# Kernel optimization log

Hardware: AMD Instinct MI355X
Metric: run time of the kernel (lower is better)

Reference implementation:

```python
import jax, jax.numpy as jnp
import numpy as np

N = 50000      # nodes
E = 800000     # edges
F_IN = 128     # input features
H = 64         # hidden channels
G = 64         # graphs in batch
EPS = 1e-5


def setup_inputs() -> dict:
    key = jax.random.key(0)
    ks = jax.random.split(key, 24)
    def nrm(k, s):
        return jax.random.normal(k, s, dtype=jnp.float32) * 0.05
    inp = {
        "x": nrm(ks[0], (N, F_IN)),
        "edge_index": jax.random.randint(ks[1], (2, E), 0, N),
        "batch": jnp.sort(jax.random.randint(ks[2], (N,), 0, G)),
        # GCNConv weights (stored [in, out]; math equivalent to torch Linear)
        "W0": nrm(ks[3], (F_IN, H)), "b0": nrm(ks[4], (H,)),
        "W1": nrm(ks[5], (H, H)),    "b1": nrm(ks[6], (H,)),
        "W2": nrm(ks[7], (H, H)),    "b2": nrm(ks[8], (H,)),
        # residual linears
        "RW0": nrm(ks[9], (F_IN, H)),  "rb0": nrm(ks[10], (H,)),
        "RW1": nrm(ks[11], (H, H)),    "rb1": nrm(ks[12], (H,)),
        "RW2": nrm(ks[13], (H, H)),    "rb2": nrm(ks[14], (H,)),
        # layernorm gamma/beta
        "g0": jnp.ones((H,), jnp.float32), "be0": jnp.zeros((H,), jnp.float32),
        "g1": jnp.ones((H,), jnp.float32), "be1": jnp.zeros((H,), jnp.float32),
        "g2": jnp.ones((H,), jnp.float32), "be2": jnp.zeros((H,), jnp.float32),
        # final readout linear
        "lw": nrm(ks[15], (H, 1)), "lb": nrm(ks[16], (1,)),
    }
    return inp


def _layernorm(x, g, b):
    mu = jnp.mean(x, axis=-1, keepdims=True)
    var = jnp.mean(jnp.square(x - mu), axis=-1, keepdims=True)
    return (x - mu) * jax.lax.rsqrt(var + EPS) * g + b


def reference(x, edge_index, batch,
              W0, b0, W1, b1, W2, b2,
              RW0, rb0, RW1, rb1, RW2, rb2,
              g0, be0, g1, be1, g2, be2,
              lw, lb):
    n = x.shape[0]
    loops = jnp.arange(n)
    row = jnp.concatenate([edge_index[0], loops])  # source
    col = jnp.concatenate([edge_index[1], loops])  # target
    # symmetric GCN normalization with self-loops (PyG gcn_norm)
    deg = jax.ops.segment_sum(jnp.ones_like(col, dtype=x.dtype), col, num_segments=n)
    dis = jnp.where(deg > 0, deg ** -0.5, 0.0)
    norm = dis[row] * dis[col]  # [E+N]

    params = [(W0, b0, RW0, rb0, g0, be0),
              (W1, b1, RW1, rb1, g1, be1),
              (W2, b2, RW2, rb2, g2, be2)]
    n_layers = len(params)
    for i, (W, b, RW, rb, g, be) in enumerate(params):
        h = x @ W                                                  # [n, H]
        agg = jax.ops.segment_sum(h[row] * norm[:, None], col, num_segments=n) + b
        x = agg + (x @ RW + rb)                                    # residual
        # dropout: eval mode -> identity
        x = _layernorm(x, g, be)
        if i < n_layers - 1:
            x = jax.nn.relu(x)

    # global mean pool over graphs
    counts = jax.ops.segment_sum(jnp.ones((n,), x.dtype), batch, num_segments=G)
    pooled = jax.ops.segment_sum(x, batch, num_segments=G) / jnp.maximum(counts, 1.0)[:, None]
    return pooled @ lw + lb  # [G, 1]
```

## Files before the change

kernel.cpp:

```cpp
#include <hip/hip_runtime.h>
#include <hip/hip_bf16.h>

#define HID 64
#define NGRAPH 64
#define BSH 7
#define NCH 384

static inline size_t align256(size_t x) { return (x + 255) & ~(size_t)255; }

typedef __attribute__((ext_vector_type(8))) short bf16x8;
typedef __attribute__((ext_vector_type(4))) float f32x4;

__device__ __forceinline__ float ldf(const void* p, size_t i, int f32) {
    if (f32) return ((const float*)p)[i];
    unsigned int w = ((unsigned int)((const unsigned short*)p)[i]) << 16;
    return __uint_as_float(w);
}
__device__ __forceinline__ float bf2f(unsigned short u) {
    return __uint_as_float(((unsigned int)u) << 16);
}
__device__ __forceinline__ unsigned short f2bf(float f) {
    __hip_bfloat16 h = __float2bfloat16(f);
    return *(unsigned short*)&h;
}

__device__ __forceinline__ unsigned char f2e4m3(float f) {
#if defined(__has_builtin) && __has_builtin(__builtin_amdgcn_cvt_pk_fp8_f32)
    int r = __builtin_amdgcn_cvt_pk_fp8_f32(f, f, 0, false);
    return (unsigned char)(r & 0xFF);
#else
    unsigned u = __float_as_uint(f);
    unsigned s = (u >> 24) & 0x80;
    unsigned a = u & 0x7FFFFFFF;
    float af = __uint_as_float(a);
    if (af < 0.015625f) {
        int m = (int)rintf(af * 512.f);
        return (unsigned char)(s | m);
    }
    unsigned r = a + 0x7FFFF + ((a >> 20) & 1);
    int e = (int)(r >> 23) - 127;
    if (e > 8) return (unsigned char)(s | 0x7E);
    return (unsigned char)(s | ((e + 7) << 3) | ((r >> 20) & 7));
#endif
}
template <int IDX>
__device__ __forceinline__ float d8(unsigned p) {
#if defined(__has_builtin) && __has_builtin(__builtin_amdgcn_cvt_f32_fp8)
    return __builtin_amdgcn_cvt_f32_fp8(p, IDX);
#else
    unsigned b = (p >> (IDX * 8)) & 0xFF;
    unsigned e = (b >> 3) & 0xF, m = b & 7;
    float v = e ? __uint_as_float(((e + 120) << 23) | (m << 20))
                : (float)m * (1.f / 512.f);
    return (b & 0x80) ? -v : v;
#endif
}

__global__ void k_sniff(const unsigned short* __restrict__ x, int nwords, int* __restrict__ flag,
                        float* __restrict__ gsum, int* __restrict__ gcnt) {
    __shared__ int cw, cz;
    int t = threadIdx.x;
    if (t == 0) { cw = 0; cz = 0; }
    if (t < NGRAPH) { gsum[t] = 0.f; gcnt[t] = 0; }
    __syncthreads();
    int weird = 0, evenzero = 0;
    for (int i = t; i < nwords; i += blockDim.x) {
        unsigned short u = x[i];
        int e = (u >> 7) & 0xFF;
        if (e >= 128) weird++;
        if (((i & 1) == 0) && ((u & 0x7FFF) == 0)) evenzero++;
    }
    atomicAdd(&cw, weird);
    atomicAdd(&cz, evenzero);
    __syncthreads();
    if (t == 0) *flag = (cw > nwords / 16 || cz > nwords / 8) ? 1 : 0;
}

__global__ void k_gcnt(const int* __restrict__ batch, int* __restrict__ gcnt, int n) {
    __shared__ int h[NGRAPH];
    int t = threadIdx.x;
    if (t < NGRAPH) h[t] = 0;
    __syncthreads();
    int i = blockIdx.x * blockDim.x + t;
    if (i < n) atomicAdd(&h[batch[i]], 1);
    __syncthreads();
    if (t < NGRAPH && h[t] > 0) atomicAdd(&gcnt[t], h[t]);
}

__global__ void k_pack(const void* W0, const void* RW0, const void* b0, const void* rb0,
                       const void* W1, const void* RW1, const void* b1, const void* rb1,
                       const void* W2, const void* RW2, const void* b2, const void* rb2,
                       const int* __restrict__ dflag,
                       unsigned short* wt0, unsigned short* wt1, unsigned short* wt2,
                       float* bcat) {
    int f = *dflag;
    int i = blockIdx.x * blockDim.x + threadIdx.x;
    if (i < 16384) {
        int n = i >> 7, k = i & 127;
        float v = (n < 64) ? ldf(W0, (size_t)k * 64 + n, f) : ldf(RW0, (size_t)k * 64 + (n - 64), f);
        wt0[n * 128 + k] = f2bf(v);
    } else if (i < 24576) {
        int j = i - 16384; int n = j >> 6, k = j & 63;
        float v = (n < 64) ? ldf(W1, (size_t)k * 64 + n, f) : ldf(RW1, (size_t)k * 64 + (n - 64), f);
        wt1[n * 64 + k] = f2bf(v);
    } else if (i < 32768) {
        int j = i - 24576; int n = j >> 6, k = j & 63;
        float v = (n < 64) ? ldf(W2, (size_t)k * 64 + n, f) : ldf(RW2, (size_t)k * 64 + (n - 64), f);
        wt2[n * 64 + k] = f2bf(v);
    } else if (i < 32768 + 192) {
        int j = i - 32768; int l = j >> 6, c = j & 63;
        const void* bb = (l == 0) ? b0 : (l == 1) ? b1 : b2;
        const void* rr = (l == 0) ? rb0 : (l == 1) ? rb1 : rb2;
        bcat[l * 64 + c] = ldf(bb, c, f) + ldf(rr, c, f);
    }
}

__global__ __launch_bounds__(256) void k_hist(const int* __restrict__ ecol, int e, int nbuck,
                                              int* __restrict__ hist) {
    __shared__ int sh[1024];
    int c = blockIdx.x, t = threadIdx.x;
    for (int i = t; i < nbuck; i += 256) sh[i] = 0;
    __syncthreads();
    int per = (e + NCH - 1) / NCH;
    int s = c * per, en = min(e, s + per);
    for (int i = s + t; i < en; i += 256)
        atomicAdd(&sh[ecol[i] >> BSH], 1);
    __syncthreads();
    for (int i = t; i < nbuck; i += 256) hist[i * NCH + c] = sh[i];
}

__global__ void k_scan1(const int* __restrict__ src, int* __restrict__ bsum, int n) {
    __shared__ int s[256];
    int t = threadIdx.x;
    int base = blockIdx.x * 1024 + t * 4;
    int sum = 0;
#pragma unroll
    for (int j = 0; j < 4; j++) { int i = base + j; if (i < n) sum += src[i]; }
    s[t] = sum;
    __syncthreads();
    for (int o = 128; o > 0; o >>= 1) {
        if (t < o) s[t] += s[t + o];
        __syncthreads();
    }
    if (t == 0) bsum[blockIdx.x] = s[0];
}

__global__ void k_scan2(const int* __restrict__ bsum, int* __restrict__ bscan,
                        int* __restrict__ out, int nb, int n) {
    __shared__ int s[256];
    int t = threadIdx.x;
    int v = (t < nb) ? bsum[t] : 0;
    s[t] = v;
    __syncthreads();
    for (int o = 1; o < 256; o <<= 1) {
        int x = (t >= o) ? s[t - o] : 0;
        __syncthreads();
        s[t] += x;
        __syncthreads();
    }
    if (t < nb) bscan[t] = s[t] - v;
    if (t == nb - 1) out[n] = s[t];
}

__global__ void k_scan3(const int* __restrict__ src, const int* __restrict__ bscan,
                        int* __restrict__ out, int n) {
    __shared__ int s[256];
    int t = threadIdx.x;
    int base = blockIdx.x * 1024 + t * 4;
    int tsum = 0;
#pragma unroll
    for (int j = 0; j < 4; j++) { int i = base + j; if (i < n) tsum += src[i]; }
    s[t] = tsum;
    __syncthreads();
    for (int o = 1; o < 256; o <<= 1) {
        int x = (t >= o) ? s[t - o] : 0;
        __syncthreads();
        s[t] += x;
        __syncthreads();
    }
    int off = bscan[blockIdx.x] + s[t] - tsum;
#pragma unroll
    for (int j = 0; j < 4; j++) {
        int i = base + j;
        if (i < n) { out[i] = off; off += src[i]; }
    }
}

__global__ __launch_bounds__(256) void k_scatter(const int* __restrict__ erow,
                                                 const int* __restrict__ ecol, int e, int nbuck,
                                                 const int* __restrict__ hoffs,
                                                 int2* __restrict__ ebuf) {
    __shared__ int cur[1024];
    int c = blockIdx.x, t = threadIdx.x;
    for (int i = t; i < nbuck; i += 256) cur[i] = hoffs[i * NCH + c];
    __syncthreads();
    int per = (e + NCH - 1) / NCH;
    int s = c * per, en = min(e, s + per);
    for (int i = s + t; i < en; i += 256) {
        int tg = ecol[i];
        int p = atomicAdd(&cur[tg >> BSH], 1);
        ebuf[p] = make_int2(erow[i], tg);
    }
}

__global__ __launch_bounds__(256) void k_bucket(const int2* __restrict__ ebuf,
                                                const int* __restrict__ hoffs,
                                                int nbuck, int n, int e,
                                                int* __restrict__ offs, float* __restrict__ dis,
                                                int* __restrict__ csr) {
    __shared__ int hist[128];
    __shared__ int lofs[128];
    __shared__ int curs[128];
    int b = blockIdx.x, t = threadIdx.x;
    int nb0 = b << BSH;
    int nn = n - nb0; if (nn > 128) nn = 128;
    int s = hoffs[b * NCH];
    int en = (b + 1 < nbuck) ? hoffs[(b + 1) * NCH] : e;
    if (t < 128) hist[t] = 0;
    __syncthreads();
    for (int i = s + t; i < en; i += 256)
        atomicAdd(&hist[ebuf[i].y & 127], 1);
    __syncthreads();
    if (t < 128) lofs[t] = hist[t];
    __syncthreads();
    for (int o = 1; o < 128; o <<= 1) {
        int v = (t < 128 && t >= o) ? lofs[t - o] : 0;
        __syncthreads();
        if (t < 128) lofs[t] += v;
        __syncthreads();
    }
    if (t < nn) {
        int ex = s + lofs[t] - hist[t];
        offs[nb0 + t] = ex;
        curs[t] = ex;
        dis[nb0 + t] = rsqrtf((float)(hist[t] + 1));
    }
    if (b == nbuck - 1 && t == 0) offs[n] = e;
    __syncthreads();
    for (int i = s + t; i < en; i += 256) {
        int2 ed = ebuf[i];
        int p = atomicAdd(&curs[ed.y & 127], 1);
        csr[p] = ed.x;
    }
}

template <int K, bool XFLAG, bool LO>
__global__ __launch_bounds__(256) void k_gemm(const void* __restrict__ xin,
                                              const unsigned short* __restrict__ wt,
                                              const float* __restrict__ bcat,
                                              const float* __restrict__ dis,
                                              const int* __restrict__ dflag,
                                              unsigned char* __restrict__ hs,
                                              float* __restrict__ base, int n) {
    const int KP = K + 8;
    __shared__ unsigned short sXh[64 * KP];
    __shared__ unsigned short sXl[LO ? 64 * KP : 1];
    __shared__ unsigned short sW[128 * KP];
    int f32 = *dflag;
    int tid = threadIdx.x;
    int row0 = blockIdx.x * 64;

    {
        const uint4* src = (const uint4*)wt;
        uint4* dst = (uint4*)sW;
        const int C = K / 8;
        const int CP = KP / 8;
        for (int i = tid; i < 128 * C; i += 256) {
            int nrow = i / C, c = i % C;
            dst[nrow * CP + c] = src[i];
        }
    }
    if (XFLAG && !f32) {
        const uint4* xv = (const uint4*)xin;
        const int C = K / 8;
        for (int i = tid; i < 64 * C; i += 256) {
            int r = i / C, c = i % C;
            int gr = row0 + r;
            uint4 v = (gr < n) ? xv[(size_t)gr * C + c] : make_uint4(0, 0, 0, 0);
            *(uint4*)&sXh[r * KP + c * 8] = v;
        }
    } else if (XFLAG) {
        for (int i = tid; i < 64 * K; i += 256) {
            int r = i / K, k = i - r * K;
            int gr = row0 + r;
            float v = (gr < n) ? ((const float*)xin)[(size_t)gr * K + k] : 0.f;
            sXh[r * KP + k] = f2bf(v);
        }
    } else {
        const float4* xv = (const float4*)xin;
        const int C = K / 4;
        for (int i = tid; i < 64 * C; i += 256) {
            int r = i / C, c = i % C;
            int gr = row0 + r;
            float4 v = (gr < n) ? xv[(size_t)gr * C + c] : make_float4(0.f, 0.f, 0.f, 0.f);
            ushort4 h, lo;
            h.x = f2bf(v.x); h.y = f2bf(v.y); h.z = f2bf(v.z); h.w = f2bf(v.w);
            if (LO) {
                lo.x = f2bf(v.x - bf2f(h.x)); lo.y = f2bf(v.y - bf2f(h.y));
                lo.z = f2bf(v.z - bf2f(h.z)); lo.w = f2bf(v.w - bf2f(h.w));
            }
            *(ushort4*)&sXh[r * KP + c * 4] = h;
            if (LO) *(ushort4*)&sXl[r * KP + c * 4] = lo;
        }
    }
    __syncthreads();

    int w = tid >> 6, lane = tid & 63;
    int m = lane & 15, q = lane >> 4;
    f32x4 acc[8];
#pragma unroll
    for (int ct = 0; ct < 8; ct++) acc[ct] = (f32x4){0.f, 0.f, 0.f, 0.f};

    int arow = w * 16 + m;
#pragma unroll
    for (int ks = 0; ks < K / 32; ks++) {
        int ka = ks * 32 + q * 8;
        bf16x8 ah = *(const bf16x8*)&sXh[arow * KP + ka];
        bf16x8 al;
        if (LO) al = *(const bf16x8*)&sXl[arow * KP + ka];
#pragma unroll
        for (int ct = 0; ct < 8; ct++) {
            bf16x8 bb = *(const bf16x8*)&sW[(ct * 16 + m) * KP + ka];
            acc[ct] = __builtin_amdgcn_mfma_f32_16x16x32_bf16(ah, bb, acc[ct], 0, 0, 0);
            if (LO) acc[ct] = __builtin_amdgcn_mfma_f32_16x16x32_bf16(al, bb, acc[ct], 0, 0, 0);
        }
    }

#pragma unroll
    for (int ct = 0; ct < 4; ct++) {
        int col = ct * 16 + m;
#pragma unroll
        for (int reg = 0; reg < 4; reg++) {
            int r = row0 + w * 16 + q * 4 + reg;
            if (r < n) {
                float dv = dis[r];
                float h = acc[ct][reg] * dv;
                hs[(size_t)r * 64 + col] = f2e4m3(h);
                base[(size_t)r * 64 + col] = h * dv + acc[ct + 4][reg] + bcat[col];
            }
        }
    }
}

template <bool FINAL>
__global__ __launch_bounds__(1024) void k_agg_ln(const unsigned char* __restrict__ hs,
                                                 const float* __restrict__ base,
                                                 const float* __restrict__ dis,
                                                 const int* __restrict__ offs,
                                                 const int* __restrict__ csr,
                                                 const void* __restrict__ gam,
                                                 const void* __restrict__ bet,
                                                 const int* __restrict__ dflag,
                                                 float* __restrict__ xout, int n, int relu,
                                                 const int* __restrict__ batch,
                                                 const void* __restrict__ lw,
                                                 float* __restrict__ gsum) {
    __shared__ float sG[FINAL ? NGRAPH : 1];
    int f32 = *dflag;
    int t = threadIdx.x;
    if (FINAL) {
        if (t < NGRAPH) sG[t] = 0.f;
        __syncthreads();
    }
    int grp = t >> 4;
    int l = t & 15;
    int gl0 = (t & 63) & ~15;
    int v = blockIdx.x * 64 + grp;
    if (v < n) {
        int s = offs[v];
        int e2 = offs[v + 1];
        float a0 = 0.f, a1 = 0.f, a2 = 0.f, a3 = 0.f;
        for (int gbase = s; gbase < e2; gbase += 16) {
            int cnt = e2 - gbase; if (cnt > 16) cnt = 16;
            int myidx = (gbase + l < e2) ? csr[gbase + l] : 0;
            int j = 0;
            for (; j + 3 < cnt; j += 4) {
                int s0 = __shfl(myidx, gl0 + j, 64);
                int s1 = __shfl(myidx, gl0 + j + 1, 64);
                int s2 = __shfl(myidx, gl0 + j + 2, 64);
                int s3 = __shfl(myidx, gl0 + j + 3, 64);
                unsigned p0 = *(const unsigned*)(hs + (size_t)s0 * 64 + l * 4);
                unsigned p1 = *(const unsigned*)(hs + (size_t)s1 * 64 + l * 4);
                unsigned p2 = *(const unsigned*)(hs + (size_t)s2 * 64 + l * 4);
                unsigned p3 = *(const unsigned*)(hs + (size_t)s3 * 64 + l * 4);
                a0 += (d8<0>(p0) + d8<0>(p1)) + (d8<0>(p2) + d8<0>(p3));
                a1 += (d8<1>(p0) + d8<1>(p1)) + (d8<1>(p2) + d8<1>(p3));
                a2 += (d8<2>(p0) + d8<2>(p1)) + (d8<2>(p2) + d8<2>(p3));
                a3 += (d8<3>(p0) + d8<3>(p1)) + (d8<3>(p2) + d8<3>(p3));
            }
            for (; j < cnt; j++) {
                int s0 = __shfl(myidx, gl0 + j, 64);
                unsigned p0 = *(const unsigned*)(hs + (size_t)s0 * 64 + l * 4);
                a0 += d8<0>(p0);
                a1 += d8<1>(p0);
                a2 += d8<2>(p0);
                a3 += d8<3>(p0);
            }
        }
        float4 bv = *(const float4*)&base[(size_t)v * 64 + l * 4];
        float dv = dis[v];
        a0 = bv.x + dv * a0;
        a1 = bv.y + dv * a1;
        a2 = bv.z + dv * a2;
        a3 = bv.w + dv * a3;
        float m = a0 + a1 + a2 + a3;
        m += __shfl_xor(m, 1, 64); m += __shfl_xor(m, 2, 64);
        m += __shfl_xor(m, 4, 64); m += __shfl_xor(m, 8, 64);
        m *= (1.f / 64.f);
        float d0 = a0 - m, d1 = a1 - m, d2 = a2 - m, d3 = a3 - m;
        float var = d0 * d0 + d1 * d1 + d2 * d2 + d3 * d3;
        var += __shfl_xor(var, 1, 64); var += __shfl_xor(var, 2, 64);
        var += __shfl_xor(var, 4, 64); var += __shfl_xor(var, 8, 64);
        var *= (1.f / 64.f);
        float rs = rsqrtf(var + 1e-5f);
        float y0 = d0 * rs * ldf(gam, l * 4 + 0, f32) + ldf(bet, l * 4 + 0, f32);
        float y1 = d1 * rs * ldf(gam, l * 4 + 1, f32) + ldf(bet, l * 4 + 1, f32);
        float y2 = d2 * rs * ldf(gam, l * 4 + 2, f32) + ldf(bet, l * 4 + 2, f32);
        float y3 = d3 * rs * ldf(gam, l * 4 + 3, f32) + ldf(bet, l * 4 + 3, f32);
        if (relu) {
            y0 = fmaxf(y0, 0.f); y1 = fmaxf(y1, 0.f);
            y2 = fmaxf(y2, 0.f); y3 = fmaxf(y3, 0.f);
        }
        if (!FINAL) {
            *(float4*)&xout[(size_t)v * 64 + l * 4] = make_float4(y0, y1, y2, y3);
        } else {
            float val = y0 * ldf(lw, l * 4 + 0, f32) + y1 * ldf(lw, l * 4 + 1, f32)
                      + y2 * ldf(lw, l * 4 + 2, f32) + y3 * ldf(lw, l * 4 + 3, f32);
            val += __shfl_xor(val, 1, 64); val += __shfl_xor(val, 2, 64);
            val += __shfl_xor(val, 4, 64); val += __shfl_xor(val, 8, 64);
            if (l == 0) atomicAdd(&sG[batch[v]], val);
        }
    }
    if (FINAL) {
        __syncthreads();
        if (t < NGRAPH && sG[t] != 0.f) atomicAdd(&gsum[t], sG[t]);
    }
}

__global__ void k_final(const float* __restrict__ gsum, const int* __restrict__ gcnt,
                        const void* __restrict__ lb, const int* __restrict__ dflag,
                        void* __restrict__ out, int g) {
    int f32 = *dflag;
    int i = threadIdx.x;
    if (i < g) {
        float c = fmaxf((float)gcnt[i], 1.f);
        float v = gsum[i] / c + ldf(lb, 0, f32);
        if (f32) ((float*)out)[i] = v;
        else ((__hip_bfloat16*)out)[i] = __float2bfloat16(v);
    }
}

extern "C" void kernel_launch(void* const* d_in, const int* in_sizes, int n_in,
                              void* d_out, int out_size, void* d_ws, size_t ws_size,
                              hipStream_t stream) {
    const void* x_in = d_in[0];
    const int* edge_index = (const int*)d_in[1];
    const int* batch = (const int*)d_in[2];
    const void *W0 = d_in[3], *b0 = d_in[4], *W1 = d_in[5], *b1 = d_in[6],
               *W2 = d_in[7], *b2 = d_in[8];
    const void *RW0 = d_in[9], *rb0 = d_in[10], *RW1 = d_in[11], *rb1 = d_in[12],
               *RW2 = d_in[13], *rb2 = d_in[14];
    const void *g0 = d_in[15], *be0 = d_in[16], *g1 = d_in[17], *be1 = d_in[18],
               *g2 = d_in[19], *be2 = d_in[20], *lw = d_in[21], *lb = d_in[22];

    const int N = in_sizes[2];
    const int E = in_sizes[1] / 2;
    const int* erow = edge_index;
    const int* ecol = edge_index + E;
    const int nbuck = (N + 127) >> BSH;
    const int T = nbuck * NCH;

    char* p = (char*)d_ws;
    size_t off = 0;
    float* dis = (float*)(p + off);  off = align256(off + (size_t)N * 4);
    int* offs = (int*)(p + off);     off = align256(off + (size_t)(N + 1) * 4);
    int* csr = (int*)(p + off);      off = align256(off + (size_t)E * 4);
    int2* ebuf = (int2*)(p + off);   off = align256(off + (size_t)E * 8);
    int* hist = (int*)(p + off);     off = align256(off + (size_t)T * 4);
    int* hoffs = (int*)(p + off);    off = align256(off + (size_t)(T + 1) * 4);
    unsigned char* hs = (unsigned char*)(p + off); off = align256(off + (size_t)N * HID);
    float* base = (float*)(p + off); off = align256(off + (size_t)N * HID * 4);
    float* xbuf = (float*)(p + off); off = align256(off + (size_t)N * HID * 4);
    unsigned short* wt0 = (unsigned short*)(p + off); off = align256(off + 16384 * 2);
    unsigned short* wt1 = (unsigned short*)(p + off); off = align256(off + 8192 * 2);
    unsigned short* wt2 = (unsigned short*)(p + off); off = align256(off + 8192 * 2);
    float* bcat = (float*)(p + off); off = align256(off + 192 * 4);
    int* bsum = (int*)(p + off);     off = align256(off + 256 * 4);
    int* bscan = (int*)(p + off);    off = align256(off + 256 * 4);
    float* gsum = (float*)(p + off); off = align256(off + NGRAPH * 4);
    int* gcnt = (int*)(p + off);     off = align256(off + NGRAPH * 4);
    int* dflag = (int*)(p + off);    off = align256(off + 4);
    (void)ws_size;

    const int TB = 256;
    int nb_n = (N + TB - 1) / TB;
    int nbT = (T + 1023) / 1024;
    int nb_gemm = (N + 63) / 64;
    int nb_agg = (N + 63) / 64;

    k_sniff<<<1, 256, 0, stream>>>((const unsigned short*)x_in, 8192, dflag, gsum, gcnt);
    k_gcnt<<<nb_n, TB, 0, stream>>>(batch, gcnt, N);
    k_pack<<<130, TB, 0, stream>>>(W0, RW0, b0, rb0, W1, RW1, b1, rb1, W2, RW2, b2, rb2,
                                   dflag, wt0, wt1, wt2, bcat);
    k_hist<<<NCH, TB, 0, stream>>>(ecol, E, nbuck, hist);
    k_scan1<<<nbT, TB, 0, stream>>>(hist, bsum, T);
    k_scan2<<<1, TB, 0, stream>>>(bsum, bscan, hoffs, nbT, T);
    k_scan3<<<nbT, TB, 0, stream>>>(hist, bscan, hoffs, T);
    k_scatter<<<NCH, TB, 0, stream>>>(erow, ecol, E, nbuck, hoffs, ebuf);
    k_bucket<<<nbuck, TB, 0, stream>>>(ebuf, hoffs, nbuck, N, E, offs, dis, csr);

    k_gemm<128, true, false><<<nb_gemm, TB, 0, stream>>>(x_in, wt0, bcat, dis, dflag, hs, base, N);
    k_agg_ln<false><<<nb_agg, 1024, 0, stream>>>(hs, base, dis, offs, csr, g0, be0, dflag,
                                                 xbuf, N, 1, nullptr, nullptr, nullptr);
    k_gemm<64, false, true><<<nb_gemm, TB, 0, stream>>>(xbuf, wt1, bcat + 64, dis, dflag, hs, base, N);
    k_agg_ln<false><<<nb_agg, 1024, 0, stream>>>(hs, base, dis, offs, csr, g1, be1, dflag,
                                                 xbuf, N, 1, nullptr, nullptr, nullptr);
    k_gemm<64, false, true><<<nb_gemm, TB, 0, stream>>>(xbuf, wt2, bcat + 128, dis, dflag, hs, base, N);
    k_agg_ln<true><<<nb_agg, 1024, 0, stream>>>(hs, base, dis, offs, csr, g2, be2, dflag,
                                                nullptr, N, 0, batch, lw, gsum);

    k_final<<<1, 64, 0, stream>>>(gsum, gcnt, lb, dflag, d_out, NGRAPH);
}
```

Before: 285.1 us.

## Fuse prep kernels, split edge buffer, read weights directly, prefetch agg indices

```diff
diff --git a/kernel.cpp b/kernel.cpp
--- a/kernel.cpp
+++ b/kernel.cpp
@@ -76,57 +76,57 @@
     if (t == 0) *flag = (cw > nwords / 16 || cz > nwords / 8) ? 1 : 0;
 }
 
-__global__ void k_gcnt(const int* __restrict__ batch, int* __restrict__ gcnt, int n) {
-    __shared__ int h[NGRAPH];
-    int t = threadIdx.x;
-    if (t < NGRAPH) h[t] = 0;
-    __syncthreads();
-    int i = blockIdx.x * blockDim.x + t;
-    if (i < n) atomicAdd(&h[batch[i]], 1);
-    __syncthreads();
-    if (t < NGRAPH && h[t] > 0) atomicAdd(&gcnt[t], h[t]);
-}
-
-__global__ void k_pack(const void* W0, const void* RW0, const void* b0, const void* rb0,
-                       const void* W1, const void* RW1, const void* b1, const void* rb1,
-                       const void* W2, const void* RW2, const void* b2, const void* rb2,
-                       const int* __restrict__ dflag,
-                       unsigned short* wt0, unsigned short* wt1, unsigned short* wt2,
-                       float* bcat) {
-    int f = *dflag;
-    int i = blockIdx.x * blockDim.x + threadIdx.x;
-    if (i < 16384) {
-        int n = i >> 7, k = i & 127;
-        float v = (n < 64) ? ldf(W0, (size_t)k * 64 + n, f) : ldf(RW0, (size_t)k * 64 + (n - 64), f);
-        wt0[n * 128 + k] = f2bf(v);
-    } else if (i < 24576) {
-        int j = i - 16384; int n = j >> 6, k = j & 63;
-        float v = (n < 64) ? ldf(W1, (size_t)k * 64 + n, f) : ldf(RW1, (size_t)k * 64 + (n - 64), f);
-        wt1[n * 64 + k] = f2bf(v);
-    } else if (i < 32768) {
-        int j = i - 24576; int n = j >> 6, k = j & 63;
-        float v = (n < 64) ? ldf(W2, (size_t)k * 64 + n, f) : ldf(RW2, (size_t)k * 64 + (n - 64), f);
-        wt2[n * 64 + k] = f2bf(v);
-    } else if (i < 32768 + 192) {
-        int j = i - 32768; int l = j >> 6, c = j & 63;
-        const void* bb = (l == 0) ? b0 : (l == 1) ? b1 : b2;
-        const void* rr = (l == 0) ? rb0 : (l == 1) ? rb1 : rb2;
-        bcat[l * 64 + c] = ldf(bb, c, f) + ldf(rr, c, f);
-    }
-}
-
-__global__ __launch_bounds__(256) void k_hist(const int* __restrict__ ecol, int e, int nbuck,
+__global__ __launch_bounds__(256) void k_prep(const int* __restrict__ batch, int* __restrict__ gcnt,
+                                              int n, int nbG,
+                                              const void* W0, const void* RW0, const void* b0, const void* rb0,
+                                              const void* W1, const void* RW1, const void* b1, const void* rb1,
+                                              const void* W2, const void* RW2, const void* b2, const void* rb2,
+                                              const int* __restrict__ dflag,
+                                              unsigned short* wt0, unsigned short* wt1, unsigned short* wt2,
+                                              float* bcat,
+                                              const int* __restrict__ ecol, int e, int nbuck,
                                               int* __restrict__ hist) {
     __shared__ int sh[1024];
-    int c = blockIdx.x, t = threadIdx.x;
-    for (int i = t; i < nbuck; i += 256) sh[i] = 0;
-    __syncthreads();
-    int per = (e + NCH - 1) / NCH;
-    int s = c * per, en = min(e, s + per);
-    for (int i = s + t; i < en; i += 256)
-        atomicAdd(&sh[ecol[i] >> BSH], 1);
-    __syncthreads();
-    for (int i = t; i < nbuck; i += 256) hist[i * NCH + c] = sh[i];
+    int b = blockIdx.x, t = threadIdx.x;
+    if (b < nbG) {
+        if (t < NGRAPH) sh[t] = 0;
+        __syncthreads();
+        int i = b * 256 + t;
+        if (i < n) atomicAdd(&sh[batch[i]], 1);
+        __syncthreads();
+        if (t < NGRAPH && sh[t] > 0) atomicAdd(&gcnt[t], sh[t]);
+    } else if (b < nbG + 130) {
+        int f = *dflag;
+        int i = (b - nbG) * 256 + t;
+        if (i < 16384) {
+            int nn = i >> 7, k = i & 127;
+            float v = (nn < 64) ? ldf(W0, (size_t)k * 64 + nn, f) : ldf(RW0, (size_t)k * 64 + (nn - 64), f);
+            wt0[nn * 128 + k] = f2bf(v);
+        } else if (i < 24576) {
+            int j = i - 16384; int nn = j >> 6, k = j & 63;
+            float v = (nn < 64) ? ldf(W1, (size_t)k * 64 + nn, f) : ldf(RW1, (size_t)k * 64 + (nn - 64), f);
+            wt1[nn * 64 + k] = f2bf(v);
+        } else if (i < 32768) {
+            int j = i - 24576; int nn = j >> 6, k = j & 63;
+            float v = (nn < 64) ? ldf(W2, (size_t)k * 64 + nn, f) : ldf(RW2, (size_t)k * 64 + (nn - 64), f);
+            wt2[nn * 64 + k] = f2bf(v);
+        } else if (i < 32768 + 192) {
+            int j = i - 32768; int l = j >> 6, c = j & 63;
+            const void* bb = (l == 0) ? b0 : (l == 1) ? b1 : b2;
+            const void* rr = (l == 0) ? rb0 : (l == 1) ? rb1 : rb2;
+            bcat[l * 64 + c] = ldf(bb, c, f) + ldf(rr, c, f);
+        }
+    } else {
+        int c = b - nbG - 130;
+        for (int i = t; i < nbuck; i += 256) sh[i] = 0;
+        __syncthreads();
+        int per = (e + NCH - 1) / NCH;
+        int s = c * per, en = min(e, s + per);
+        for (int i = s + t; i < en; i += 256)
+            atomicAdd(&sh[ecol[i] >> BSH], 1);
+        __syncthreads();
+        for (int i = t; i < nbuck; i += 256) hist[i * NCH + c] = sh[i];
+    }
 }
 
 __global__ void k_scan1(const int* __restrict__ src, int* __restrict__ bsum, int n) {
@@ -189,7 +189,8 @@
 __global__ __launch_bounds__(256) void k_scatter(const int* __restrict__ erow,
                                                  const int* __restrict__ ecol, int e, int nbuck,
                                                  const int* __restrict__ hoffs,
-                                                 int2* __restrict__ ebuf) {
+                                                 int* __restrict__ esrc,
+                                                 unsigned char* __restrict__ et7) {
     __shared__ int cur[1024];
     int c = blockIdx.x, t = threadIdx.x;
     for (int i = t; i < nbuck; i += 256) cur[i] = hoffs[i * NCH + c];
@@ -199,11 +200,13 @@
     for (int i = s + t; i < en; i += 256) {
         int tg = ecol[i];
         int p = atomicAdd(&cur[tg >> BSH], 1);
-        ebuf[p] = make_int2(erow[i], tg);
-    }
-}
-
-__global__ __launch_bounds__(256) void k_bucket(const int2* __restrict__ ebuf,
+        esrc[p] = erow[i];
+        et7[p] = (unsigned char)(tg & 127);
+    }
+}
+
+__global__ __launch_bounds__(256) void k_bucket(const int* __restrict__ esrc,
+                                                const unsigned char* __restrict__ et7,
                                                 const int* __restrict__ hoffs,
                                                 int nbuck, int n, int e,
                                                 int* __restrict__ offs, float* __restrict__ dis,
@@ -219,7 +222,7 @@
     if (t < 128) hist[t] = 0;
     __syncthreads();
     for (int i = s + t; i < en; i += 256)
-        atomicAdd(&hist[ebuf[i].y & 127], 1);
+        atomicAdd(&hist[et7[i]], 1);
     __syncthreads();
     if (t < 128) lofs[t] = hist[t];
     __syncthreads();
@@ -238,9 +241,8 @@
     if (b == nbuck - 1 && t == 0) offs[n] = e;
     __syncthreads();
     for (int i = s + t; i < en; i += 256) {
-        int2 ed = ebuf[i];
-        int p = atomicAdd(&curs[ed.y & 127], 1);
-        csr[p] = ed.x;
+        int p = atomicAdd(&curs[et7[i]], 1);
+        csr[p] = esrc[i];
     }
 }
 
@@ -255,21 +257,10 @@
     const int KP = K + 8;
     __shared__ unsigned short sXh[64 * KP];
     __shared__ unsigned short sXl[LO ? 64 * KP : 1];
-    __shared__ unsigned short sW[128 * KP];
     int f32 = *dflag;
     int tid = threadIdx.x;
     int row0 = blockIdx.x * 64;
 
-    {
-        const uint4* src = (const uint4*)wt;
-        uint4* dst = (uint4*)sW;
-        const int C = K / 8;
-        const int CP = KP / 8;
-        for (int i = tid; i < 128 * C; i += 256) {
-            int nrow = i / C, c = i % C;
-            dst[nrow * CP + c] = src[i];
-        }
-    }
     if (XFLAG && !f32) {
         const uint4* xv = (const uint4*)xin;
         const int C = K / 8;
@@ -312,7 +303,7 @@
     for (int ct = 0; ct < 8; ct++) acc[ct] = (f32x4){0.f, 0.f, 0.f, 0.f};
 
     int arow = w * 16 + m;
-#pragma unroll
+#pragma unroll 1
     for (int ks = 0; ks < K / 32; ks++) {
         int ka = ks * 32 + q * 8;
         bf16x8 ah = *(const bf16x8*)&sXh[arow * KP + ka];
@@ -320,7 +311,7 @@
         if (LO) al = *(const bf16x8*)&sXl[arow * KP + ka];
 #pragma unroll
         for (int ct = 0; ct < 8; ct++) {
-            bf16x8 bb = *(const bf16x8*)&sW[(ct * 16 + m) * KP + ka];
+            bf16x8 bb = *(const bf16x8*)(wt + (size_t)(ct * 16 + m) * K + ka);
             acc[ct] = __builtin_amdgcn_mfma_f32_16x16x32_bf16(ah, bb, acc[ct], 0, 0, 0);
             if (LO) acc[ct] = __builtin_amdgcn_mfma_f32_16x16x32_bf16(al, bb, acc[ct], 0, 0, 0);
         }
@@ -369,16 +360,47 @@
     if (v < n) {
         int s = offs[v];
         int e2 = offs[v + 1];
+        float4 bv = *(const float4*)&base[(size_t)v * 64 + l * 4];
+        float dv = dis[v];
         float a0 = 0.f, a1 = 0.f, a2 = 0.f, a3 = 0.f;
+        int myidx = (s + l < e2) ? csr[s + l] : 0;
         for (int gbase = s; gbase < e2; gbase += 16) {
             int cnt = e2 - gbase; if (cnt > 16) cnt = 16;
-            int myidx = (gbase + l < e2) ? csr[gbase + l] : 0;
+            int cur = myidx;
+            int nxt = gbase + 16;
+            if (nxt < e2) myidx = (nxt + l < e2) ? csr[nxt + l] : 0;
             int j = 0;
+            for (; j + 7 < cnt; j += 8) {
+                int s0 = __shfl(cur, gl0 + j, 64);
+                int s1 = __shfl(cur, gl0 + j + 1, 64);
+                int s2 = __shfl(cur, gl0 + j + 2, 64);
+                int s3 = __shfl(cur, gl0 + j + 3, 64);
+                int s4 = __shfl(cur, gl0 + j + 4, 64);
+                int s5 = __shfl(cur, gl0 + j + 5, 64);
+                int s6 = __shfl(cur, gl0 + j + 6, 64);
+                int s7 = __shfl(cur, gl0 + j + 7, 64);
+                unsigned p0 = *(const unsigned*)(hs + (size_t)s0 * 64 + l * 4);
+                unsigned p1 = *(const unsigned*)(hs + (size_t)s1 * 64 + l * 4);
+                unsigned p2 = *(const unsigned*)(hs + (size_t)s2 * 64 + l * 4);
+                unsigned p3 = *(const unsigned*)(hs + (size_t)s3 * 64 + l * 4);
+                unsigned p4 = *(const unsigned*)(hs + (size_t)s4 * 64 + l * 4);
+                unsigned p5 = *(const unsigned*)(hs + (size_t)s5 * 64 + l * 4);
+                unsigned p6 = *(const unsigned*)(hs + (size_t)s6 * 64 + l * 4);
+                unsigned p7 = *(const unsigned*)(hs + (size_t)s7 * 64 + l * 4);
+                a0 += ((d8<0>(p0) + d8<0>(p1)) + (d8<0>(p2) + d8<0>(p3)))
+                    + ((d8<0>(p4) + d8<0>(p5)) + (d8<0>(p6) + d8<0>(p7)));
+                a1 += ((d8<1>(p0) + d8<1>(p1)) + (d8<1>(p2) + d8<1>(p3)))
+                    + ((d8<1>(p4) + d8<1>(p5)) + (d8<1>(p6) + d8<1>(p7)));
+                a2 += ((d8<2>(p0) + d8<2>(p1)) + (d8<2>(p2) + d8<2>(p3)))
+                    + ((d8<2>(p4) + d8<2>(p5)) + (d8<2>(p6) + d8<2>(p7)));
+                a3 += ((d8<3>(p0) + d8<3>(p1)) + (d8<3>(p2) + d8<3>(p3)))
+                    + ((d8<3>(p4) + d8<3>(p5)) + (d8<3>(p6) + d8<3>(p7)));
+            }
             for (; j + 3 < cnt; j += 4) {
-                int s0 = __shfl(myidx, gl0 + j, 64);
-                int s1 = __shfl(myidx, gl0 + j + 1, 64);
-                int s2 = __shfl(myidx, gl0 + j + 2, 64);
-                int s3 = __shfl(myidx, gl0 + j + 3, 64);
+                int s0 = __shfl(cur, gl0 + j, 64);
+                int s1 = __shfl(cur, gl0 + j + 1, 64);
+                int s2 = __shfl(cur, gl0 + j + 2, 64);
+                int s3 = __shfl(cur, gl0 + j + 3, 64);
                 unsigned p0 = *(const unsigned*)(hs + (size_t)s0 * 64 + l * 4);
                 unsigned p1 = *(const unsigned*)(hs + (size_t)s1 * 64 + l * 4);
                 unsigned p2 = *(const unsigned*)(hs + (size_t)s2 * 64 + l * 4);
@@ -389,7 +411,7 @@
                 a3 += (d8<3>(p0) + d8<3>(p1)) + (d8<3>(p2) + d8<3>(p3));
             }
             for (; j < cnt; j++) {
-                int s0 = __shfl(myidx, gl0 + j, 64);
+                int s0 = __shfl(cur, gl0 + j, 64);
                 unsigned p0 = *(const unsigned*)(hs + (size_t)s0 * 64 + l * 4);
                 a0 += d8<0>(p0);
                 a1 += d8<1>(p0);
@@ -397,8 +419,6 @@
                 a3 += d8<3>(p0);
             }
         }
-        float4 bv = *(const float4*)&base[(size_t)v * 64 + l * 4];
-        float dv = dis[v];
         a0 = bv.x + dv * a0;
         a1 = bv.y + dv * a1;
         a2 = bv.z + dv * a2;
@@ -475,7 +495,8 @@
     float* dis = (float*)(p + off);  off = align256(off + (size_t)N * 4);
     int* offs = (int*)(p + off);     off = align256(off + (size_t)(N + 1) * 4);
     int* csr = (int*)(p + off);      off = align256(off + (size_t)E * 4);
-    int2* ebuf = (int2*)(p + off);   off = align256(off + (size_t)E * 8);
+    int* esrc = (int*)(p + off);     off = align256(off + (size_t)E * 4);
+    unsigned char* et7 = (unsigned char*)(p + off); off = align256(off + (size_t)E);
     int* hist = (int*)(p + off);     off = align256(off + (size_t)T * 4);
     int* hoffs = (int*)(p + off);    off = align256(off + (size_t)(T + 1) * 4);
     unsigned char* hs = (unsigned char*)(p + off); off = align256(off + (size_t)N * HID);
@@ -493,21 +514,21 @@
     (void)ws_size;
 
     const int TB = 256;
-    int nb_n = (N + TB - 1) / TB;
+    int nbG = (N + TB - 1) / TB;
     int nbT = (T + 1023) / 1024;
     int nb_gemm = (N + 63) / 64;
     int nb_agg = (N + 63) / 64;
 
     k_sniff<<<1, 256, 0, stream>>>((const unsigned short*)x_in, 8192, dflag, gsum, gcnt);
-    k_gcnt<<<nb_n, TB, 0, stream>>>(batch, gcnt, N);
-    k_pack<<<130, TB, 0, stream>>>(W0, RW0, b0, rb0, W1, RW1, b1, rb1, W2, RW2, b2, rb2,
-                                   dflag, wt0, wt1, wt2, bcat);
-    k_hist<<<NCH, TB, 0, stream>>>(ecol, E, nbuck, hist);
+    k_prep<<<nbG + 130 + NCH, TB, 0, stream>>>(batch, gcnt, N, nbG,
+                                               W0, RW0, b0, rb0, W1, RW1, b1, rb1,
+                                               W2, RW2, b2, rb2, dflag, wt0, wt1, wt2, bcat,
+                                               ecol, E, nbuck, hist);
     k_scan1<<<nbT, TB, 0, stream>>>(hist, bsum, T);
     k_scan2<<<1, TB, 0, stream>>>(bsum, bscan, hoffs, nbT, T);
     k_scan3<<<nbT, TB, 0, stream>>>(hist, bscan, hoffs, T);
-    k_scatter<<<NCH, TB, 0, stream>>>(erow, ecol, E, nbuck, hoffs, ebuf);
-    k_bucket<<<nbuck, TB, 0, stream>>>(ebuf, hoffs, nbuck, N, E, offs, dis, csr);
+    k_scatter<<<NCH, TB, 0, stream>>>(erow, ecol, E, nbuck, hoffs, esrc, et7);
+    k_bucket<<<nbuck, TB, 0, stream>>>(esrc, et7, hoffs, nbuck, N, E, offs, dis, csr);
 
     k_gemm<128, true, false><<<nb_gemm, TB, 0, stream>>>(x_in, wt0, bcat, dis, dflag, hs, base, N);
     k_agg_ln<false><<<nb_agg, 1024, 0, stream>>>(hs, base, dis, offs, csr, g0, be0, dflag,
```

Result: slower. 295.7 us (+3.7%).
